# Kernel tuning notes

Hardware: AMD Instinct MI355X
Metric: run time of the kernel (lower is better)

Reference implementation:

```python
import jax, jax.numpy as jnp
import numpy as np

K_SIZE = 41
N = 33554433  # 2**25 + 1; odd so (K_SIZE - N) is even and padded length == K_SIZE


def setup_inputs() -> dict:
    key = jax.random.key(0)
    x = jax.random.normal(key, (N,), dtype=jnp.float32)
    scale = jnp.asarray(10.0, dtype=jnp.float32)  # learned parameter self.scale
    return {"input": x, "scale": scale}


def reference(input, scale):
    n = input.shape[0]
    # z_i = linspace(-k_size//2 + 1, k_size//2, k_size) = -20 .. 20
    z = jnp.linspace(-20.0, 20.0, K_SIZE).astype(input.dtype)
    # flat structuring element: 0 inside |z| <= scale, -inf outside
    h = jnp.where(jnp.abs(z) <= scale, jnp.float32(0.0), jnp.float32(-jnp.inf))
    # F.pad(input, (missing//2+2, missing//2-2)) with missing = K_SIZE - n:
    # negative pads crop, yielding a length-K_SIZE window at static offset a.
    missing = K_SIZE - n
    a = -(missing // 2 + 2)  # Python floor-div matches torch semantics
    padded = input[a:a + K_SIZE]  # [K_SIZE]
    # out[x] = max_j( padded[(j + x) % K] + h[j] ); torch.roll is periodic,
    # so out is periodic in x with period K_SIZE. Compute the K_SIZE base
    # values once, then gather — identical math, no O(n*K) intermediate.
    j = jnp.arange(K_SIZE)
    M = padded[(j[:, None] + j[None, :]) % K_SIZE] + h[None, :]  # [K, K]
    base = jnp.max(M, axis=1)  # [K_SIZE]
    return base[jnp.arange(n) % K_SIZE]  # [n]
```

## Files before the change

kernel.cpp:

```cpp
#include <hip/hip_runtime.h>
#include <math.h>

#define K_SIZE 41

__global__ void __launch_bounds__(256)
FlatDilation1D_kernel(const float* __restrict__ in,
                      const float* __restrict__ scale_p,
                      float* __restrict__ out,
                      long long n, long long a, long long n4) {
    __shared__ float s_pad[K_SIZE];
    __shared__ float s_ext[K_SIZE + 3];

    const int tid = threadIdx.x;

    if (tid < K_SIZE) {
        s_pad[tid] = in[a + tid];
    }
    __syncthreads();

    if (tid < K_SIZE) {
        const float scale = *scale_p;
        float m = -INFINITY;
        #pragma unroll
        for (int j = 0; j < K_SIZE; ++j) {
            const float z = -20.0f + (float)j;
            if (fabsf(z) <= scale) {
                int idx = tid + j;
                if (idx >= K_SIZE) idx -= K_SIZE;
                m = fmaxf(m, s_pad[idx]);
            }
        }
        s_ext[tid] = m;
    }
    __syncthreads();
    if (tid < 3) {
        s_ext[K_SIZE + tid] = s_ext[tid];
    }
    __syncthreads();

    const long long q = (long long)blockIdx.x * blockDim.x + tid;
    if (q < n4) {
        const unsigned int r = (4u * (unsigned int)q) % 41u;
        float4 v;
        v.x = s_ext[r];
        v.y = s_ext[r + 1];
        v.z = s_ext[r + 2];
        v.w = s_ext[r + 3];
        reinterpret_cast<float4*>(out)[q] = v;
    }

    if (blockIdx.x == 0) {
        const long long tail_start = n4 * 4;
        const long long k = tail_start + tid;
        if (k < n) {
            out[k] = s_ext[(unsigned int)(k % K_SIZE)];
        }
    }
}

extern "C" void kernel_launch(void* const* d_in, const int* in_sizes, int n_in,
                              void* d_out, int out_size, void* d_ws, size_t ws_size,
                              hipStream_t stream) {
    const float* in      = (const float*)d_in[0];
    const float* scale_p = (const float*)d_in[1];
    float* out           = (float*)d_out;

    const long long n = (long long)in_sizes[0];

    const long long missing = (long long)K_SIZE - n;
    long long fd = missing / 2;
    if ((missing % 2 != 0) && (missing < 0)) fd -= 1;
    const long long a = -(fd + 2);

    const long long n4 = n / 4;
    const int block = 256;
    const long long grid = (n4 + block - 1) / block;

    FlatDilation1D_kernel<<<(dim3)(unsigned int)grid, block, 0, stream>>>(
        in, scale_p, out, n, a, n4);
}
```

Before: 217.5 us.

## Split into pattern kernel and coalesced float4 store kernel

The change computes the 41-entry periodic pattern once, in a single small kernel, and writes it to workspace as 41 float4 values. A second kernel loads the pattern into shared memory and has each thread write 16 float4s with a strided residue update, which removes the per-block recomputation of the dilation and the per-element modulo. In exchange it adds a second kernel launch and a serial tail loop in one thread.

After: 206.2 us. 5.2% less time.

```diff
diff --git a/kernel.cpp b/kernel.cpp
--- a/kernel.cpp
+++ b/kernel.cpp
@@ -3,19 +3,16 @@
 
 #define K_SIZE 41
 
-__global__ void __launch_bounds__(256)
-FlatDilation1D_kernel(const float* __restrict__ in,
-                      const float* __restrict__ scale_p,
-                      float* __restrict__ out,
-                      long long n, long long a, long long n4) {
+__global__ void __launch_bounds__(64)
+FlatDilation1D_pattern_kernel(const float* __restrict__ in,
+                              const float* __restrict__ scale_p,
+                              float4* __restrict__ pat4,
+                              long long a) {
     __shared__ float s_pad[K_SIZE];
     __shared__ float s_ext[K_SIZE + 3];
-
     const int tid = threadIdx.x;
 
-    if (tid < K_SIZE) {
-        s_pad[tid] = in[a + tid];
-    }
+    if (tid < K_SIZE) s_pad[tid] = in[a + tid];
     __syncthreads();
 
     if (tid < K_SIZE) {
@@ -33,27 +30,53 @@
         s_ext[tid] = m;
     }
     __syncthreads();
-    if (tid < 3) {
-        s_ext[K_SIZE + tid] = s_ext[tid];
-    }
+    if (tid < 3) s_ext[K_SIZE + tid] = s_ext[tid];
     __syncthreads();
 
-    const long long q = (long long)blockIdx.x * blockDim.x + tid;
-    if (q < n4) {
-        const unsigned int r = (4u * (unsigned int)q) % 41u;
+    if (tid < K_SIZE) {
+        const unsigned int r = (4u * (unsigned int)tid) % 41u;
         float4 v;
         v.x = s_ext[r];
         v.y = s_ext[r + 1];
         v.z = s_ext[r + 2];
         v.w = s_ext[r + 3];
-        reinterpret_cast<float4*>(out)[q] = v;
+        pat4[tid] = v;
+    }
+}
+
+#define S2_BLOCK 256
+#define STORES_PER_THREAD 16
+
+__global__ void __launch_bounds__(S2_BLOCK)
+FlatDilation1D_store_kernel(const float4* __restrict__ pat4,
+                            float4* __restrict__ out4,
+                            float* __restrict__ out,
+                            long long n, long long n4) {
+    __shared__ float4 s_pat4[K_SIZE];
+    const int tid = threadIdx.x;
+
+    if (tid < K_SIZE) s_pat4[tid] = pat4[tid];
+    __syncthreads();
+
+    const long long q0 = (long long)blockIdx.x * (S2_BLOCK * STORES_PER_THREAD) + tid;
+    unsigned int r = (unsigned int)((q0) % 41u);
+    r = (unsigned int)(((unsigned long long)q0) % 41ull);
+
+    long long q = q0;
+    #pragma unroll
+    for (int t = 0; t < STORES_PER_THREAD; ++t) {
+        if (q < n4) {
+            out4[q] = s_pat4[r];
+        }
+        q += S2_BLOCK;
+        r += 10u;
+        if (r >= 41u) r -= 41u;
     }
 
-    if (blockIdx.x == 0) {
-        const long long tail_start = n4 * 4;
-        const long long k = tail_start + tid;
-        if (k < n) {
-            out[k] = s_ext[(unsigned int)(k % K_SIZE)];
+    if (blockIdx.x == 0 && tid == 0) {
+        const float* s_flat = (const float*)s_pat4;
+        for (long long k = n4 * 4; k < n; ++k) {
+            out[k] = s_flat[(unsigned int)(((unsigned long long)k) % 41ull)];
         }
     }
 }
@@ -64,6 +87,7 @@
     const float* in      = (const float*)d_in[0];
     const float* scale_p = (const float*)d_in[1];
     float* out           = (float*)d_out;
+    float4* pat4         = (float4*)d_ws;
 
     const long long n = (long long)in_sizes[0];
 
@@ -73,9 +97,11 @@
     const long long a = -(fd + 2);
 
     const long long n4 = n / 4;
-    const int block = 256;
-    const long long grid = (n4 + block - 1) / block;
 
-    FlatDilation1D_kernel<<<(dim3)(unsigned int)grid, block, 0, stream>>>(
-        in, scale_p, out, n, a, n4);
+    FlatDilation1D_pattern_kernel<<<1, 64, 0, stream>>>(in, scale_p, pat4, a);
+
+    const long long per_block = (long long)S2_BLOCK * STORES_PER_THREAD;
+    const long long grid = (n4 + per_block - 1) / per_block;
+    FlatDilation1D_store_kernel<<<(dim3)(unsigned int)grid, S2_BLOCK, 0, stream>>>(
+        pat4, (float4*)out, out, n, n4);
 }
```

## Use fixed persistent grid with period-aligned stride to reuse computed float4 pattern

Applied to the files above, without the earlier changes.

Replaces the one-thread-per-float4 launch with a fixed grid of 2050 blocks that loop over the output. The total stride in elements (4*256*2050) is a multiple of 41, so each thread computes its float4 of periodic values once and stores the same vector on every iteration. This cuts the per-block prologue (gathering the window, computing 41 maxima, three barriers) from tens of thousands of blocks down to 2050. In exchange there are fewer blocks to hide store latency, and the few tail elements are now written serially by a single thread.

Result: faster. 202.6 us (-6.8%).

```diff
diff --git a/kernel.cpp b/kernel.cpp
--- a/kernel.cpp
+++ b/kernel.cpp
@@ -2,22 +2,23 @@
 #include <math.h>
 
 #define K_SIZE 41
+#define BLOCK 256
+#define GRID 2050
+#define STRIDE ((long long)BLOCK * GRID)
 
-__global__ void __launch_bounds__(256)
+__global__ void __launch_bounds__(BLOCK)
 FlatDilation1D_kernel(const float* __restrict__ in,
                       const float* __restrict__ scale_p,
+                      float4* __restrict__ out4,
                       float* __restrict__ out,
-                      long long n, long long a, long long n4) {
+                      long long n, long long n4, long long a,
+                      int full_iters) {
     __shared__ float s_pad[K_SIZE];
     __shared__ float s_ext[K_SIZE + 3];
-
     const int tid = threadIdx.x;
 
-    if (tid < K_SIZE) {
-        s_pad[tid] = in[a + tid];
-    }
+    if (tid < K_SIZE) s_pad[tid] = in[a + tid];
     __syncthreads();
-
     if (tid < K_SIZE) {
         const float scale = *scale_p;
         float m = -INFINITY;
@@ -33,27 +34,29 @@
         s_ext[tid] = m;
     }
     __syncthreads();
-    if (tid < 3) {
-        s_ext[K_SIZE + tid] = s_ext[tid];
-    }
+    if (tid < 3) s_ext[K_SIZE + tid] = s_ext[tid];
     __syncthreads();
 
-    const long long q = (long long)blockIdx.x * blockDim.x + tid;
-    if (q < n4) {
-        const unsigned int r = (4u * (unsigned int)q) % 41u;
-        float4 v;
-        v.x = s_ext[r];
-        v.y = s_ext[r + 1];
-        v.z = s_ext[r + 2];
-        v.w = s_ext[r + 3];
-        reinterpret_cast<float4*>(out)[q] = v;
+    long long q = (long long)blockIdx.x * BLOCK + tid;
+    const unsigned int r = (4u * (unsigned int)q) % 41u;
+    float4 v;
+    v.x = s_ext[r];
+    v.y = s_ext[r + 1];
+    v.z = s_ext[r + 2];
+    v.w = s_ext[r + 3];
+
+    for (int it = 0; it < full_iters; ++it) {
+        out4[q] = v;
+        q += STRIDE;
+    }
+    while (q < n4) {
+        out4[q] = v;
+        q += STRIDE;
     }
 
-    if (blockIdx.x == 0) {
-        const long long tail_start = n4 * 4;
-        const long long k = tail_start + tid;
-        if (k < n) {
-            out[k] = s_ext[(unsigned int)(k % K_SIZE)];
+    if (blockIdx.x == 0 && tid == 0) {
+        for (long long k = n4 * 4; k < n; ++k) {
+            out[k] = s_ext[(unsigned int)(((unsigned long long)k) % 41ull)];
         }
     }
 }
@@ -73,9 +76,8 @@
     const long long a = -(fd + 2);
 
     const long long n4 = n / 4;
-    const int block = 256;
-    const long long grid = (n4 + block - 1) / block;
+    const int full_iters = (int)(n4 / STRIDE);
 
-    FlatDilation1D_kernel<<<(dim3)(unsigned int)grid, block, 0, stream>>>(
-        in, scale_p, out, n, a, n4);
+    FlatDilation1D_kernel<<<GRID, BLOCK, 0, stream>>>(
+        in, scale_p, (float4*)out, out, n, n4, a, full_iters);
 }
```
